# Performance work log

Hardware: AMD Instinct MI355X
Metric: run time of the kernel (lower is better)

The kernel has to match this reference:

```python
import jax, jax.numpy as jnp
import numpy as np

EPS = 1e-8  # torch.nn.CosineSimilarity default eps


def setup_inputs() -> dict:
    key = jax.random.key(0)
    ks = jax.random.split(key, 6)
    B, N, SD, HD, AD = 512, 256, 1024, 512, 256
    return {
        "state_emb": jax.random.normal(ks[0], (B, SD), dtype=jnp.float32),
        "hints_emb": jax.random.normal(ks[1], (B, N, HD), dtype=jnp.float32),
        "Ws": jax.random.normal(ks[2], (AD, SD), dtype=jnp.float32) * 0.02,
        "bs": jax.random.normal(ks[3], (AD,), dtype=jnp.float32) * 0.02,
        "Wh": jax.random.normal(ks[4], (AD, HD), dtype=jnp.float32) * 0.02,
        "bh": jax.random.normal(ks[5], (AD,), dtype=jnp.float32) * 0.02,
    }


def reference(state_emb, hints_emb, Ws, bs, Wh, bh):
    # Projections
    sp = state_emb @ Ws.T + bs                       # (B, A)
    hp = jnp.einsum("bnh,ah->bna", hints_emb, Wh) + bh  # (B, N, A)
    # Cosine similarity along feature dim (torch CosineSimilarity semantics)
    sn = jnp.maximum(jnp.linalg.norm(sp, axis=-1, keepdims=True), EPS)    # (B,1)
    hn = jnp.maximum(jnp.linalg.norm(hp, axis=-1), EPS)                   # (B,N)
    scores = jnp.einsum("ba,bna->bn", sp, hp) / (sn * hn)                 # (B,N)
    attn_weights = jax.nn.softmax(scores, axis=1)                         # (B,N)
    # Weighted sum over hints (original, unprojected embeddings)
    output = jnp.einsum("bn,bnh->bh", attn_weights, hints_emb)            # (B,HD)
    return output
```

## Files before the change

### kernel.cpp

```cpp
#include <hip/hip_runtime.h>
#include <hip/hip_bf16.h>

typedef __attribute__((ext_vector_type(8))) short bf16x8;
typedef __attribute__((ext_vector_type(4))) float f32x4;

#define B_  512
#define N_  256
#define SD_ 1024
#define HD_ 512
#define AD_ 256

__device__ __forceinline__ unsigned short f2bf(float f) {
    unsigned int u = __float_as_uint(f);
    unsigned int r = (u + 0x7FFFu + ((u >> 16) & 1u)) >> 16;
    return (unsigned short)r;
}

__global__ void k0_pack(const float* __restrict__ Wh, unsigned short* __restrict__ whp) {
    int g = blockIdx.x * 256 + threadIdx.x;
    int ct  = g >> 10;
    int rem = g & 1023;
    int ks  = rem >> 6;
    int l   = rem & 63;
    int a   = ct * 16 + (l & 15);
    int kb  = ks * 32 + (l >> 4) * 8;
    const float* src = Wh + (size_t)a * HD_ + kb;
    float4 v0 = *(const float4*)(src);
    float4 v1 = *(const float4*)(src + 4);
    bf16x8 o;
    o[0] = (short)f2bf(v0.x); o[1] = (short)f2bf(v0.y);
    o[2] = (short)f2bf(v0.z); o[3] = (short)f2bf(v0.w);
    o[4] = (short)f2bf(v1.x); o[5] = (short)f2bf(v1.y);
    o[6] = (short)f2bf(v1.z); o[7] = (short)f2bf(v1.w);
    ((bf16x8*)whp)[g] = o;
}

__global__ __launch_bounds__(512) void k1_proj(
    const float* __restrict__ state, const float* __restrict__ Ws,
    const float* __restrict__ bs, const float* __restrict__ Wh,
    const float* __restrict__ bh,
    float* __restrict__ sn, float* __restrict__ qv, float* __restrict__ cv)
{
    __shared__ float st[2][SD_];
    __shared__ float spl[2][AD_];
    __shared__ float red[2][AD_];
    int tid = threadIdx.x, lane = tid & 63, w = tid >> 6;
    int b0 = blockIdx.x * 2;
    ((float4*)st)[tid] = ((const float4*)(state + (size_t)b0 * SD_))[tid];
    __syncthreads();
    float4 s0[4], s1[4];
    #pragma unroll
    for (int seg = 0; seg < 4; ++seg) {
        s0[seg] = *(const float4*)&st[0][seg * 256 + lane * 4];
        s1[seg] = *(const float4*)&st[1][seg * 256 + lane * 4];
    }
    #pragma unroll 2
    for (int i = 0; i < 32; ++i) {
        int a = w * 32 + i;
        const float4* wr = (const float4*)(Ws + (size_t)a * SD_);
        float p0 = 0.f, p1 = 0.f;
        #pragma unroll
        for (int seg = 0; seg < 4; ++seg) {
            float4 wv = wr[seg * 64 + lane];
            p0 += wv.x * s0[seg].x + wv.y * s0[seg].y + wv.z * s0[seg].z + wv.w * s0[seg].w;
            p1 += wv.x * s1[seg].x + wv.y * s1[seg].y + wv.z * s1[seg].z + wv.w * s1[seg].w;
        }
        #pragma unroll
        for (int d = 1; d < 64; d <<= 1) { p0 += __shfl_xor(p0, d); p1 += __shfl_xor(p1, d); }
        if (lane == 0) {
            float bsa = bs[a];
            spl[0][a] = p0 + bsa;
            spl[1][a] = p1 + bsa;
        }
    }
    __syncthreads();
    int tb = tid >> 8, t = tid & 255;
    float sv = spl[tb][t];
    red[tb][t] = sv * sv;
    __syncthreads();
    for (int s = 128; s > 0; s >>= 1) { if (t < s) red[tb][t] += red[tb][t + s]; __syncthreads(); }
    if (t == 0) sn[b0 + tb] = fmaxf(sqrtf(red[tb][0]), 1e-8f);
    __syncthreads();
    red[tb][t] = sv * bh[t];
    __syncthreads();
    for (int s = 128; s > 0; s >>= 1) { if (t < s) red[tb][t] += red[tb][t + s]; __syncthreads(); }
    if (t == 0) cv[b0 + tb] = red[tb][0];
    float q0 = 0.f, q1 = 0.f;
    #pragma unroll 8
    for (int a = 0; a < AD_; ++a) {
        float wv = Wh[(size_t)a * HD_ + tid];
        q0 += spl[0][a] * wv;
        q1 += spl[1][a] * wv;
    }
    qv[(size_t)b0 * HD_ + tid] = q0;
    qv[(size_t)(b0 + 1) * HD_ + tid] = q1;
}

__device__ __forceinline__ void stage_write(
    unsigned short* Ab, const float4* v, int row, int q4, int kc,
    float& num_reg, const float* q_lds)
{
    #pragma unroll
    for (int j = 0; j < 8; ++j) {
        int kl = q4 * 32 + j * 4;
        float4 qq = *(const float4*)(q_lds + kc * 128 + kl);
        float4 x = v[j];
        num_reg += x.x * qq.x + x.y * qq.y + x.z * qq.z + x.w * qq.w;
        ushort4 u;
        u.x = f2bf(x.x); u.y = f2bf(x.y); u.z = f2bf(x.z); u.w = f2bf(x.w);
        *(ushort4*)((char*)Ab + row * 256 + ((kl * 2) ^ ((row & 7) << 4))) = u;
    }
}

__global__ __launch_bounds__(512, 2) void k2_fused(
    const float* __restrict__ hints, const unsigned short* __restrict__ whp,
    const float* __restrict__ qv, const float* __restrict__ cv,
    const float* __restrict__ sn, const float* __restrict__ bh,
    float* __restrict__ out)
{
    __shared__ unsigned short A_bf[2][128 * 128];
    __shared__ float q_lds[HD_];
    __shared__ float bh_lds[AD_];
    __shared__ float norm2p[8][128];
    __shared__ float num_lds[128][4];
    __shared__ float sc[N_];
    __shared__ float red[N_];
    __shared__ float wsm[N_];

    int tid = threadIdx.x, lane = tid & 63, w = tid >> 6;
    int b = blockIdx.x;
    const float* hb = hints + (size_t)b * N_ * HD_;
    if (tid < 128) ((float4*)q_lds)[tid] = ((const float4*)(qv + (size_t)b * HD_))[tid];
    else if (tid < 192) ((float4*)bh_lds)[tid - 128] = ((const float4*)bh)[tid - 128];
    float cvb = cv[b];
    float snb = sn[b];
    int row = tid >> 2, q4 = tid & 3;
    __syncthreads();

    for (int mc = 0; mc < 2; ++mc) {
        f32x4 acc[8][2];
        #pragma unroll
        for (int mf = 0; mf < 8; ++mf) {
            acc[mf][0] = (f32x4){0.f, 0.f, 0.f, 0.f};
            acc[mf][1] = (f32x4){0.f, 0.f, 0.f, 0.f};
        }
        float num_reg = 0.f;
        const float* arow = hb + (size_t)(mc * 128 + row) * HD_;
        float4 v[8];
        #pragma unroll
        for (int j = 0; j < 8; ++j) v[j] = *(const float4*)(arow + q4 * 32 + j * 4);
        stage_write(A_bf[0], v, row, q4, 0, num_reg, q_lds);
        __syncthreads();
        for (int kc = 0; kc < 4; ++kc) {
            if (kc < 3) {
                #pragma unroll
                for (int j = 0; j < 8; ++j)
                    v[j] = *(const float4*)(arow + (kc + 1) * 128 + q4 * 32 + j * 4);
            }
            const unsigned short* Ab = A_bf[kc & 1];
            int kc4 = kc * 4;
            #pragma unroll
            for (int ks = 0; ks < 4; ++ks) {
                bf16x8 bfr0 = ((const bf16x8*)whp)[((2 * w + 0) * 16 + kc4 + ks) * 64 + lane];
                bf16x8 bfr1 = ((const bf16x8*)whp)[((2 * w + 1) * 16 + kc4 + ks) * 64 + lane];
                #pragma unroll
                for (int mf = 0; mf < 8; ++mf) {
                    int r = mf * 16 + (lane & 15);
                    bf16x8 afr = *(const bf16x8*)((const char*)Ab + r * 256 +
                                 ((ks * 64 + (lane >> 4) * 16) ^ ((r & 7) << 4)));
                    acc[mf][0] = __builtin_amdgcn_mfma_f32_16x16x32_bf16(afr, bfr0, acc[mf][0], 0, 0, 0);
                    acc[mf][1] = __builtin_amdgcn_mfma_f32_16x16x32_bf16(afr, bfr1, acc[mf][1], 0, 0, 0);
                }
            }
            if (kc < 3) stage_write(A_bf[(kc + 1) & 1], v, row, q4, kc + 1, num_reg, q_lds);
            __syncthreads();
        }
        num_lds[row][q4] = num_reg;
        int q4l = lane >> 4;
        float bh0 = bh_lds[(2 * w + 0) * 16 + (lane & 15)];
        float bh1 = bh_lds[(2 * w + 1) * 16 + (lane & 15)];
        #pragma unroll
        for (int mf = 0; mf < 8; ++mf) {
            #pragma unroll
            for (int r = 0; r < 4; ++r) {
                float h0 = acc[mf][0][r] + bh0;
                float h1 = acc[mf][1][r] + bh1;
                float vv = h0 * h0 + h1 * h1;
                vv += __shfl_xor(vv, 1); vv += __shfl_xor(vv, 2);
                vv += __shfl_xor(vv, 4); vv += __shfl_xor(vv, 8);
                if ((lane & 15) == 0) norm2p[w][mf * 16 + q4l * 4 + r] = vv;
            }
        }
        __syncthreads();
        if (tid < 128) {
            float n2 = 0.f;
            #pragma unroll
            for (int ww = 0; ww < 8; ++ww) n2 += norm2p[ww][tid];
            float nm = num_lds[tid][0] + num_lds[tid][1] + num_lds[tid][2] + num_lds[tid][3];
            float hn = fmaxf(sqrtf(n2), 1e-8f);
            sc[mc * 128 + tid] = (nm + cvb) / (snb * hn);
        }
        __syncthreads();
    }

    if (tid < 256) red[tid] = sc[tid];
    __syncthreads();
    for (int s = 128; s > 0; s >>= 1) { if (tid < s) red[tid] = fmaxf(red[tid], red[tid + s]); __syncthreads(); }
    float mx = red[0];
    __syncthreads();
    if (tid < 256) { float e = __expf(sc[tid] - mx); sc[tid] = e; red[tid] = e; }
    __syncthreads();
    for (int s = 128; s > 0; s >>= 1) { if (tid < s) red[tid] += red[tid + s]; __syncthreads(); }
    float inv = 1.f / red[0];
    __syncthreads();
    if (tid < 256) wsm[tid] = sc[tid] * inv;
    __syncthreads();

    float acc_o = 0.f;
    #pragma unroll 8
    for (int n = 0; n < N_; ++n)
        acc_o += wsm[n] * hb[(size_t)n * HD_ + tid];
    out[(size_t)b * HD_ + tid] = acc_o;
}

extern "C" void kernel_launch(void* const* d_in, const int* in_sizes, int n_in,
                              void* d_out, int out_size, void* d_ws, size_t ws_size,
                              hipStream_t stream) {
    const float* state = (const float*)d_in[0];
    const float* hints = (const float*)d_in[1];
    const float* Ws    = (const float*)d_in[2];
    const float* bs    = (const float*)d_in[3];
    const float* Wh    = (const float*)d_in[4];
    const float* bh    = (const float*)d_in[5];
    float* out = (float*)d_out;

    float* sn = (float*)d_ws;
    float* cv = sn + B_;
    float* qv = cv + B_;
    unsigned short* whp = (unsigned short*)(qv + (size_t)B_ * HD_);

    k0_pack<<<64, 256, 0, stream>>>(Wh, whp);
    k1_proj<<<B_ / 2, 512, 0, stream>>>(state, Ws, bs, Wh, bh, sn, qv, cv);
    k2_fused<<<B_, 512, 0, stream>>>(hints, whp, qv, cv, sn, bh, out);
}
```

Before: 184.1 us.

## Coalesce hint loads, vectorize weighted-sum pass, raise occupancy bound

Rewires the staging loads so each warp of 32 threads reads one contiguous 512-byte row segment instead of four threads covering a whole row, which gives coalesced global reads. The q-dot partial sums are then reduced across lanes with shuffles. The final softmax-weighted sum now uses float4 loads split across four groups of hint rows, with the partials combined through a scratch area in shared memory. Shared memory moves into one manually carved buffer, and launch bounds go from 2 to 4 blocks per SM. Register pressure may rise, and the higher occupancy target can force register spills.

```diff
diff --git a/kernel.cpp b/kernel.cpp
--- a/kernel.cpp
+++ b/kernel.cpp
@@ -96,36 +96,23 @@
     qv[(size_t)(b0 + 1) * HD_ + tid] = q1;
 }
 
-__device__ __forceinline__ void stage_write(
-    unsigned short* Ab, const float4* v, int row, int q4, int kc,
-    float& num_reg, const float* q_lds)
-{
-    #pragma unroll
-    for (int j = 0; j < 8; ++j) {
-        int kl = q4 * 32 + j * 4;
-        float4 qq = *(const float4*)(q_lds + kc * 128 + kl);
-        float4 x = v[j];
-        num_reg += x.x * qq.x + x.y * qq.y + x.z * qq.z + x.w * qq.w;
-        ushort4 u;
-        u.x = f2bf(x.x); u.y = f2bf(x.y); u.z = f2bf(x.z); u.w = f2bf(x.w);
-        *(ushort4*)((char*)Ab + row * 256 + ((kl * 2) ^ ((row & 7) << 4))) = u;
-    }
-}
-
-__global__ __launch_bounds__(512, 2) void k2_fused(
+__global__ __launch_bounds__(512, 4) void k2_fused(
     const float* __restrict__ hints, const unsigned short* __restrict__ whp,
     const float* __restrict__ qv, const float* __restrict__ cv,
     const float* __restrict__ sn, const float* __restrict__ bh,
     float* __restrict__ out)
 {
-    __shared__ unsigned short A_bf[2][128 * 128];
-    __shared__ float q_lds[HD_];
-    __shared__ float bh_lds[AD_];
-    __shared__ float norm2p[8][128];
-    __shared__ float num_lds[128][4];
-    __shared__ float sc[N_];
-    __shared__ float red[N_];
-    __shared__ float wsm[N_];
+    __shared__ __align__(16) char smem[76288];
+    unsigned short* A_bf0 = (unsigned short*)smem;
+    unsigned short* A_bf1 = (unsigned short*)(smem + 32768);
+    float* q_lds   = (float*)(smem + 65536);
+    float* bh_lds  = (float*)(smem + 67584);
+    float* norm2p  = (float*)(smem + 68608);
+    float* num_lds = (float*)(smem + 72704);
+    float* sc      = (float*)(smem + 73216);
+    float* red     = (float*)(smem + 74240);
+    float* wsm     = (float*)(smem + 75264);
+    float* scratch = (float*)smem;
 
     int tid = threadIdx.x, lane = tid & 63, w = tid >> 6;
     int b = blockIdx.x;
@@ -134,7 +121,8 @@
     else if (tid < 192) ((float4*)bh_lds)[tid - 128] = ((const float4*)bh)[tid - 128];
     float cvb = cv[b];
     float snb = sn[b];
-    int row = tid >> 2, q4 = tid & 3;
+    int rr = tid >> 5;
+    int cg = tid & 31;
     __syncthreads();
 
     for (int mc = 0; mc < 2; ++mc) {
@@ -144,20 +132,35 @@
             acc[mf][0] = (f32x4){0.f, 0.f, 0.f, 0.f};
             acc[mf][1] = (f32x4){0.f, 0.f, 0.f, 0.f};
         }
-        float num_reg = 0.f;
-        const float* arow = hb + (size_t)(mc * 128 + row) * HD_;
+        float num_reg[8];
+        #pragma unroll
+        for (int j = 0; j < 8; ++j) num_reg[j] = 0.f;
+        const float* hmc = hb + (size_t)(mc * 128 + rr) * HD_ + cg * 4;
+
         float4 v[8];
         #pragma unroll
-        for (int j = 0; j < 8; ++j) v[j] = *(const float4*)(arow + q4 * 32 + j * 4);
-        stage_write(A_bf[0], v, row, q4, 0, num_reg, q_lds);
+        for (int j = 0; j < 8; ++j) v[j] = *(const float4*)(hmc + (size_t)j * 16 * HD_);
+        {
+            float4 qq = *(const float4*)(q_lds + cg * 4);
+            #pragma unroll
+            for (int j = 0; j < 8; ++j) {
+                int row = j * 16 + rr;
+                float4 x = v[j];
+                num_reg[j] += x.x * qq.x + x.y * qq.y + x.z * qq.z + x.w * qq.w;
+                ushort4 u;
+                u.x = f2bf(x.x); u.y = f2bf(x.y); u.z = f2bf(x.z); u.w = f2bf(x.w);
+                *(ushort4*)((char*)A_bf0 + row * 256 + ((cg * 8) ^ ((row & 7) << 4))) = u;
+            }
+        }
         __syncthreads();
+
         for (int kc = 0; kc < 4; ++kc) {
             if (kc < 3) {
                 #pragma unroll
                 for (int j = 0; j < 8; ++j)
-                    v[j] = *(const float4*)(arow + (kc + 1) * 128 + q4 * 32 + j * 4);
-            }
-            const unsigned short* Ab = A_bf[kc & 1];
+                    v[j] = *(const float4*)(hmc + (size_t)j * 16 * HD_ + (kc + 1) * 128);
+            }
+            const unsigned short* Ab = (kc & 1) ? A_bf1 : A_bf0;
             int kc4 = kc * 4;
             #pragma unroll
             for (int ks = 0; ks < 4; ++ks) {
@@ -172,10 +175,30 @@
                     acc[mf][1] = __builtin_amdgcn_mfma_f32_16x16x32_bf16(afr, bfr1, acc[mf][1], 0, 0, 0);
                 }
             }
-            if (kc < 3) stage_write(A_bf[(kc + 1) & 1], v, row, q4, kc + 1, num_reg, q_lds);
+            if (kc < 3) {
+                unsigned short* Aw = (kc & 1) ? A_bf0 : A_bf1;
+                float4 qq = *(const float4*)(q_lds + (kc + 1) * 128 + cg * 4);
+                #pragma unroll
+                for (int j = 0; j < 8; ++j) {
+                    int row = j * 16 + rr;
+                    float4 x = v[j];
+                    num_reg[j] += x.x * qq.x + x.y * qq.y + x.z * qq.z + x.w * qq.w;
+                    ushort4 u;
+                    u.x = f2bf(x.x); u.y = f2bf(x.y); u.z = f2bf(x.z); u.w = f2bf(x.w);
+                    *(ushort4*)((char*)Aw + row * 256 + ((cg * 8) ^ ((row & 7) << 4))) = u;
+                }
+            }
             __syncthreads();
         }
-        num_lds[row][q4] = num_reg;
+
+        #pragma unroll
+        for (int j = 0; j < 8; ++j) {
+            float nv = num_reg[j];
+            nv += __shfl_xor(nv, 1); nv += __shfl_xor(nv, 2); nv += __shfl_xor(nv, 4);
+            nv += __shfl_xor(nv, 8); nv += __shfl_xor(nv, 16);
+            if ((tid & 31) == 0) num_lds[j * 16 + rr] = nv;
+        }
+
         int q4l = lane >> 4;
         float bh0 = bh_lds[(2 * w + 0) * 16 + (lane & 15)];
         float bh1 = bh_lds[(2 * w + 1) * 16 + (lane & 15)];
@@ -188,17 +211,16 @@
                 float vv = h0 * h0 + h1 * h1;
                 vv += __shfl_xor(vv, 1); vv += __shfl_xor(vv, 2);
                 vv += __shfl_xor(vv, 4); vv += __shfl_xor(vv, 8);
-                if ((lane & 15) == 0) norm2p[w][mf * 16 + q4l * 4 + r] = vv;
+                if ((lane & 15) == 0) norm2p[w * 128 + mf * 16 + q4l * 4 + r] = vv;
             }
         }
         __syncthreads();
         if (tid < 128) {
             float n2 = 0.f;
             #pragma unroll
-            for (int ww = 0; ww < 8; ++ww) n2 += norm2p[ww][tid];
-            float nm = num_lds[tid][0] + num_lds[tid][1] + num_lds[tid][2] + num_lds[tid][3];
+            for (int ww = 0; ww < 8; ++ww) n2 += norm2p[ww * 128 + tid];
             float hn = fmaxf(sqrtf(n2), 1e-8f);
-            sc[mc * 128 + tid] = (nm + cvb) / (snb * hn);
+            sc[mc * 128 + tid] = (num_lds[tid] + cvb) / (snb * hn);
         }
         __syncthreads();
     }
@@ -216,11 +238,19 @@
     if (tid < 256) wsm[tid] = sc[tid] * inv;
     __syncthreads();
 
-    float acc_o = 0.f;
+    int hg = tid & 127, ng = tid >> 7;
+    const float* hbe = hb + (size_t)(ng * 64) * HD_ + hg * 4;
+    float ax = 0.f, ay = 0.f, az = 0.f, aw = 0.f;
     #pragma unroll 8
-    for (int n = 0; n < N_; ++n)
-        acc_o += wsm[n] * hb[(size_t)n * HD_ + tid];
-    out[(size_t)b * HD_ + tid] = acc_o;
+    for (int n = 0; n < 64; ++n) {
+        float4 hv = *(const float4*)(hbe + (size_t)n * HD_);
+        float wn = wsm[ng * 64 + n];
+        ax += wn * hv.x; ay += wn * hv.y; az += wn * hv.z; aw += wn * hv.w;
+    }
+    *(float4*)(scratch + ng * 512 + hg * 4) = (float4){ax, ay, az, aw};
+    __syncthreads();
+    out[(size_t)b * HD_ + tid] =
+        scratch[tid] + scratch[512 + tid] + scratch[1024 + tid] + scratch[1536 + tid];
 }
 
 extern "C" void kernel_launch(void* const* d_in, const int* in_sizes, int n_in,
```

Measured after the change: 353.3 us. 1.92x slower.
